# Kernel tuning notes

Hardware: AMD Instinct MI355X
Metric: run time of the kernel (lower is better)

The kernel has to match this reference:

```python
import jax, jax.numpy as jnp
import numpy as np

EMBED_DIM = 1024
BATCH = 4
SEQ = 2048


def setup_inputs() -> dict:
    key = jax.random.key(0)
    ks = jax.random.split(key, 9)
    E = EMBED_DIM
    s = 1.0 / np.sqrt(E)
    inp = {
        "x": jax.random.normal(ks[0], (BATCH, SEQ, E), dtype=jnp.float32),
        "Wq": jax.random.uniform(ks[1], (E, E), jnp.float32, -s, s),
        "bq": jax.random.uniform(ks[2], (E,), jnp.float32, -s, s),
        "Wk": jax.random.uniform(ks[3], (E, E), jnp.float32, -s, s),
        "bk": jax.random.uniform(ks[4], (E,), jnp.float32, -s, s),
        "Wv": jax.random.uniform(ks[5], (E, E), jnp.float32, -s, s),
        "bv": jax.random.uniform(ks[6], (E,), jnp.float32, -s, s),
        "Wo": jax.random.uniform(ks[7], (E, E), jnp.float32, -s, s),
        "bo": jax.random.uniform(ks[8], (E,), jnp.float32, -s, s),
    }
    return inp


def reference(x, Wq, bq, Wk, bk, Wv, bv, Wo, bo):
    # x: [B, S, E]. Single-head attention over full embed_dim.
    scale = x.shape[-1] ** -0.5
    q = jnp.einsum("bse,ef->bsf", x, Wq.T) + bq
    k = jnp.einsum("bse,ef->bsf", x, Wk.T) + bk
    v = jnp.einsum("bse,ef->bsf", x, Wv.T) + bv
    scores = jnp.einsum("bqe,bke->bqk", q, k) * scale  # [B, S, S]
    attn = jax.nn.softmax(scores, axis=-1)             # dropout p=0 -> identity
    out = jnp.einsum("bqk,bke->bqe", attn, v)
    return jnp.einsum("bse,ef->bsf", out, Wo.T) + bo
```

## Files before the change

kernel.cpp:

```cpp
#include <hip/hip_runtime.h>
#include <hip/hip_bf16.h>


typedef __bf16 bf16_t;
typedef __bf16 bf16x8 __attribute__((ext_vector_type(8)));
typedef __bf16 bf16x4 __attribute__((ext_vector_type(4)));
typedef float  f32x16 __attribute__((ext_vector_type(16)));
typedef float  f32x4  __attribute__((ext_vector_type(4)));

__device__ __forceinline__ void async_copy16(const void* g, void* l) {
  __builtin_amdgcn_global_load_lds(
      (const __attribute__((address_space(1))) void*)g,
      (__attribute__((address_space(3))) void*)l, 16, 0, 0);
}

__device__ __forceinline__ void wg_barrier() {
  asm volatile("" ::: "memory");
  __builtin_amdgcn_s_barrier();
  asm volatile("" ::: "memory");
}

__device__ __forceinline__ unsigned lds_addr(const void* p) {
  return (unsigned)(unsigned long long)(__attribute__((address_space(3))) const void*)p;
}

__device__ __forceinline__ bf16x8 ds_read128(const bf16_t* p) {
  bf16x8 r;
  asm volatile("ds_read_b128 %0, %1" : "=v"(r) : "v"(lds_addr(p)));
  return r;
}

__device__ __forceinline__ f32x4 mfma16(bf16x8 a, bf16x8 b, f32x4 c) {
  return __builtin_amdgcn_mfma_f32_16x16x32_bf16(a, b, c, 0, 0, 0);
}

__device__ __forceinline__ void store_out(float* p, float v)  { *p = v; }
__device__ __forceinline__ void store_out(bf16_t* p, float v) { *p = (bf16_t)v; }

#define BM 128
#define BN 128
#define BKT 64

template <typename OutT, int NBIAS>
__global__ __launch_bounds__(512, 2) void gemm256_bt(
    const bf16_t* __restrict__ A, const bf16_t* __restrict__ B,
    OutT* __restrict__ C,
    const float* __restrict__ b0, const float* __restrict__ b1,
    const float* __restrict__ b2,
    int M, int N, int K, int lda, int ldb, int ldc, float scale,
    long long strideA, long long strideB, long long strideC) {
  const int z = blockIdx.z;
  A += (long long)z * strideA;
  B += (long long)z * strideB;
  C += (long long)z * strideC;

  int bx = blockIdx.x, by = blockIdx.y;
  {
    const int GX  = gridDim.x;
    const int id  = by * GX + bx;
    const int per = GX * 8;
    const int grp = id / per;
    const int rem = id - grp * per;
    by = grp * 8 + (rem & 7);
    bx = rem >> 3;
  }

  __shared__ __align__(16) bf16_t As[2 * 256 * 64];
  __shared__ __align__(16) bf16_t Bs[2 * 256 * 64];

  const int t    = threadIdx.x;
  const int lane = t & 63;
  const int w    = t >> 6;
  const int wm   = w & 1;
  const int wn   = w >> 1;
  const int g    = lane >> 4;
  const int l7   = lane & 7;
  const int r15  = lane & 15;
  const int tileM = by * 256;
  const int tileN = bx * 256;

  const int row0 = t >> 3;
  const int gcc  = (t & 7) ^ (row0 & 7);
  const int dstb = (t & ~63) * 8;

  const int sw0 = ((0 + g) ^ l7) * 8;
  const int sw1 = ((4 + g) ^ l7) * 8;
  const int aRow = (wm * 128 + r15) * 64;
  const int bRow = (wn * 64 + r15) * 64;

  const int NT = K >> 6;

  f32x4 acc[8][4] = {};

  auto stageA = [&](int kt, int h) {
    const int cb = (kt & 1) * 16384;
    const bf16_t* src =
        A + (long long)(tileM + h * 128 + row0) * lda + kt * 64 + gcc * 8;
    bf16_t* dst = &As[cb + h * 8192 + dstb];
    async_copy16(src, dst);
    async_copy16(src + (long long)64 * lda, dst + 4096);
  };
  auto stageB = [&](int kt, int h) {
    const int cb = (kt & 1) * 16384;
    const bf16_t* src =
        B + (long long)(tileN + h * 128 + row0) * ldb + kt * 64 + gcc * 8;
    bf16_t* dst = &Bs[cb + h * 8192 + dstb];
    async_copy16(src, dst);
    async_copy16(src + (long long)64 * ldb, dst + 4096);
  };

  stageA(0, 0); stageA(0, 1); stageB(0, 0); stageB(0, 1);
  stageA(1, 0); stageA(1, 1); stageB(1, 0); stageB(1, 1);
  asm volatile("s_waitcnt vmcnt(8)" ::: "memory");
  wg_barrier();

  bf16x8 a[4][2], bq[2][2][2];

  for (int kt = 0; kt < NT; ++kt) {
    const int cb = (kt & 1) * 16384;
    const int k2 = kt + 2;
    const bf16_t* Ab = &As[cb + aRow];
    const bf16_t* Bb = &Bs[cb + bRow];

#pragma unroll
    for (int i = 0; i < 4; ++i) {
      a[i][0] = ds_read128(Ab + i * 1024 + sw0);
      a[i][1] = ds_read128(Ab + i * 1024 + sw1);
    }
#pragma unroll
    for (int j = 0; j < 2; ++j) {
      bq[0][j][0] = ds_read128(Bb + j * 1024 + sw0);
      bq[0][j][1] = ds_read128(Bb + j * 1024 + sw1);
    }
    wg_barrier();
    asm volatile("s_waitcnt lgkmcnt(0)");
    __builtin_amdgcn_sched_barrier(0);
    __builtin_amdgcn_s_setprio(1);
#pragma unroll
    for (int i = 0; i < 4; ++i)
#pragma unroll
      for (int j = 0; j < 2; ++j) {
        acc[i][j] = mfma16(a[i][0], bq[0][j][0], acc[i][j]);
        acc[i][j] = mfma16(a[i][1], bq[0][j][1], acc[i][j]);
      }
    __builtin_amdgcn_s_setprio(0);
    wg_barrier();

#pragma unroll
    for (int j = 0; j < 2; ++j) {
      bq[1][j][0] = ds_read128(Bb + 2048 + j * 1024 + sw0);
      bq[1][j][1] = ds_read128(Bb + 2048 + j * 1024 + sw1);
    }
    wg_barrier();
    asm volatile("s_waitcnt lgkmcnt(0)");
    __builtin_amdgcn_sched_barrier(0);
    __builtin_amdgcn_s_setprio(1);
#pragma unroll
    for (int i = 0; i < 4; ++i)
#pragma unroll
      for (int j = 0; j < 2; ++j) {
        acc[i][2 + j] = mfma16(a[i][0], bq[1][j][0], acc[i][2 + j]);
        acc[i][2 + j] = mfma16(a[i][1], bq[1][j][1], acc[i][2 + j]);
      }
    __builtin_amdgcn_s_setprio(0);
    wg_barrier();

#pragma unroll
    for (int i = 0; i < 4; ++i) {
      a[i][0] = ds_read128(Ab + 4096 + i * 1024 + sw0);
      a[i][1] = ds_read128(Ab + 4096 + i * 1024 + sw1);
    }
    if (k2 < NT) { stageB(k2, 0); stageB(k2, 1); }
    wg_barrier();
    asm volatile("s_waitcnt lgkmcnt(0)");
    __builtin_amdgcn_sched_barrier(0);
    __builtin_amdgcn_s_setprio(1);
#pragma unroll
    for (int i = 0; i < 4; ++i)
#pragma unroll
      for (int j = 0; j < 2; ++j) {
        acc[4 + i][2 + j] = mfma16(a[i][0], bq[1][j][0], acc[4 + i][2 + j]);
        acc[4 + i][2 + j] = mfma16(a[i][1], bq[1][j][1], acc[4 + i][2 + j]);
      }
    __builtin_amdgcn_s_setprio(0);
    wg_barrier();

    if (k2 < NT) { stageA(k2, 0); stageA(k2, 1); }
    __builtin_amdgcn_s_setprio(1);
#pragma unroll
    for (int i = 0; i < 4; ++i)
#pragma unroll
      for (int j = 0; j < 2; ++j) {
        acc[4 + i][j] = mfma16(a[i][0], bq[0][j][0], acc[4 + i][j]);
        acc[4 + i][j] = mfma16(a[i][1], bq[0][j][1], acc[4 + i][j]);
      }
    __builtin_amdgcn_s_setprio(0);
    if (k2 < NT) asm volatile("s_waitcnt vmcnt(8)" ::: "memory");
    else         asm volatile("s_waitcnt vmcnt(0)" ::: "memory");
    wg_barrier();
  }

  float bvv[4];
#pragma unroll
  for (int j = 0; j < 4; ++j) {
    const int col = tileN + wn * 64 + j * 16 + r15;
    float bv = 0.f;
    if (NBIAS == 1) bv = b0[col];
    if (NBIAS == 3) {
      const float* bp = col < 1024 ? b0 : (col < 2048 ? b1 : b2);
      bv = bp[col & 1023];
    }
    bvv[j] = bv;
  }
#pragma unroll
  for (int i = 0; i < 8; ++i) {
#pragma unroll
    for (int r = 0; r < 4; ++r) {
      const long long row = tileM + wm * 128 + i * 16 + g * 4 + r;
      OutT* Crow = C + row * ldc + tileN + wn * 64 + r15;
#pragma unroll
      for (int j = 0; j < 4; ++j)
        store_out(Crow + j * 16, acc[i][j][r] * scale + bvv[j]);
    }
  }
}

template <typename OutT, int NBIAS>
__global__ __launch_bounds__(256) void gemm_bt(
    const bf16_t* __restrict__ A, const bf16_t* __restrict__ B,
    OutT* __restrict__ C,
    const float* __restrict__ b0, const float* __restrict__ b1,
    const float* __restrict__ b2,
    int M, int N, int K, int lda, int ldb, int ldc, float scale,
    long long strideA, long long strideB, long long strideC) {
  const int z = blockIdx.z;
  A += (long long)z * strideA;
  B += (long long)z * strideB;
  C += (long long)z * strideC;

  int bx = blockIdx.x, by = blockIdx.y;
  {
    const int GX  = gridDim.x;
    const int id  = by * GX + bx;
    const int per = GX * 8;
    const int grp = id / per;
    const int rem = id - grp * per;
    by = grp * 8 + (rem & 7);
    bx = rem >> 3;
  }

  __shared__ __align__(16) bf16_t As[BM * BKT];
  __shared__ __align__(16) bf16_t Bs[BN * BKT];

  const int t    = threadIdx.x;
  const int lane = t & 63;
  const int w    = t >> 6;
  const int wm   = w & 1;
  const int wn   = w >> 1;
  const int tileM = by * BM;
  const int tileN = bx * BN;

  f32x16 acc[2][2] = {};

  for (int k0 = 0; k0 < K; k0 += BKT) {
#pragma unroll
    for (int i = 0; i < 4; ++i) {
      const int c   = t + 256 * i;
      const int row = c >> 3;
      const int cc  = c & 7;
      const int gcc = cc ^ (row & 7);
      const int ldsbase = ((t & ~63) + 256 * i) * 8;
      async_copy16(A + (long long)(tileM + row) * lda + k0 + gcc * 8, &As[ldsbase]);
      async_copy16(B + (long long)(tileN + row) * ldb + k0 + gcc * 8, &Bs[ldsbase]);
    }
    __syncthreads();

#pragma unroll
    for (int s = 0; s < 4; ++s) {
      const int kc = s + 4 * (lane >> 5);
      bf16x8 af[2], bfr[2];
#pragma unroll
      for (int ti = 0; ti < 2; ++ti) {
        const int row = wm * 64 + ti * 32 + (lane & 31);
        af[ti] = *(const bf16x8*)&As[row * BKT + ((kc ^ (row & 7)) * 8)];
      }
#pragma unroll
      for (int tj = 0; tj < 2; ++tj) {
        const int row = wn * 64 + tj * 32 + (lane & 31);
        bfr[tj] = *(const bf16x8*)&Bs[row * BKT + ((kc ^ (row & 7)) * 8)];
      }
#pragma unroll
      for (int ti = 0; ti < 2; ++ti)
#pragma unroll
        for (int tj = 0; tj < 2; ++tj)
          acc[ti][tj] = __builtin_amdgcn_mfma_f32_32x32x16_bf16(
              af[ti], bfr[tj], acc[ti][tj], 0, 0, 0);
    }
    __syncthreads();
  }

#pragma unroll
  for (int tj = 0; tj < 2; ++tj) {
    const int col = tileN + wn * 64 + tj * 32 + (lane & 31);
    float bv = 0.f;
    if (NBIAS == 1) bv = b0[col];
    if (NBIAS == 3) {
      const float* bp = col < 1024 ? b0 : (col < 2048 ? b1 : b2);
      bv = bp[col & 1023];
    }
#pragma unroll
    for (int ti = 0; ti < 2; ++ti) {
      const int rowb = tileM + wm * 64 + ti * 32 + 4 * (lane >> 5);
#pragma unroll
      for (int r = 0; r < 16; ++r) {
        const int row = rowb + (r & 3) + 8 * (r >> 2);
        store_out(&C[(long long)row * ldc + col], acc[ti][tj][r] * scale + bv);
      }
    }
  }
}

__global__ __launch_bounds__(256) void cast_all(
    const float4* __restrict__ w0, const float4* __restrict__ w1,
    const float4* __restrict__ w2, const float4* __restrict__ w3,
    const float4* __restrict__ x,
    bf16x4* __restrict__ wdst, bf16x4* __restrict__ xdst) {
  const int N4W = 1 << 18;
  const int id = blockIdx.x * 256 + threadIdx.x;
  const float4* src;
  bf16x4* dst;
  if (id < 4 * N4W) {
    const int z = id >> 18;
    src = (z == 0 ? w0 : z == 1 ? w1 : z == 2 ? w2 : w3) + (id & (N4W - 1));
    dst = wdst + id;
  } else {
    const int i = id - 4 * N4W;
    src = x + i;
    dst = xdst + i;
  }
  const float4 v = *src;
  bf16x4 o;
  o[0] = (bf16_t)v.x; o[1] = (bf16_t)v.y; o[2] = (bf16_t)v.z; o[3] = (bf16_t)v.w;
  *dst = o;
}

__global__ __launch_bounds__(256) void transpose_bf16(
    const bf16_t* __restrict__ in, bf16_t* __restrict__ out, int R, int C,
    int ldin, long long sIn, long long sOut) {
  in  += (long long)blockIdx.z * sIn;
  out += (long long)blockIdx.z * sOut;
  __shared__ bf16_t tile[32][33];
  const int tx = threadIdx.x, ty = threadIdx.y;
  const int x = blockIdx.x * 32 + tx;
  const int y0 = blockIdx.y * 32;
#pragma unroll
  for (int j = 0; j < 32; j += 8)
    tile[ty + j][tx] = in[(long long)(y0 + ty + j) * ldin + x];
  __syncthreads();
  const int x2 = y0 + tx;
  const int y2 = blockIdx.x * 32;
#pragma unroll
  for (int j = 0; j < 32; j += 8)
    out[(long long)(y2 + ty + j) * R + x2] = tile[tx][ty + j];
}

__global__ __launch_bounds__(256) void softmax_rows(
    const bf16_t* __restrict__ S, bf16_t* __restrict__ P, int cols) {
  const long long row = blockIdx.x;
  const bf16x8* inp = (const bf16x8*)(S + row * cols);
  bf16x8* outp      = (bf16x8*)(P + row * cols);
  const int t = threadIdx.x;
  const int w = t >> 6, lane = t & 63;

  const bf16x8 v = inp[t];
  float f[8];
#pragma unroll
  for (int j = 0; j < 8; ++j) f[j] = (float)v[j];

  float m = f[0];
#pragma unroll
  for (int j = 1; j < 8; ++j) m = fmaxf(m, f[j]);
#pragma unroll
  for (int off = 32; off > 0; off >>= 1) m = fmaxf(m, __shfl_xor(m, off));

  __shared__ float red[8];
  if (lane == 0) red[w] = m;
  __syncthreads();
  m = fmaxf(fmaxf(red[0], red[1]), fmaxf(red[2], red[3]));

  float e[8], sum = 0.f;
#pragma unroll
  for (int j = 0; j < 8; ++j) { e[j] = __expf(f[j] - m); sum += e[j]; }
#pragma unroll
  for (int off = 32; off > 0; off >>= 1) sum += __shfl_xor(sum, off);
  if (lane == 0) red[4 + w] = sum;
  __syncthreads();
  sum = red[4] + red[5] + red[6] + red[7];

  const float inv = 1.f / sum;
  bf16x8 o;
#pragma unroll
  for (int j = 0; j < 8; ++j) o[j] = (bf16_t)(e[j] * inv);
  outp[t] = o;
}

extern "C" void kernel_launch(void* const* d_in, const int* in_sizes, int n_in,
                              void* d_out, int out_size, void* d_ws, size_t ws_size,
                              hipStream_t stream) {
  const int E = 1024, S = 2048, B = 4;
  const int BS = B * S;

  const float* x  = (const float*)d_in[0];
  const float* Wq = (const float*)d_in[1];
  const float* bq = (const float*)d_in[2];
  const float* Wk = (const float*)d_in[3];
  const float* bk = (const float*)d_in[4];
  const float* Wv = (const float*)d_in[5];
  const float* bv = (const float*)d_in[6];
  const float* Wo = (const float*)d_in[7];
  const float* bo = (const float*)d_in[8];
  float* out = (float*)d_out;

  char* w = (char*)d_ws;
  const size_t MB = 1ull << 20;
  bf16_t* Wqkvb = (bf16_t*)(w + 0 * MB);
  bf16_t* Wob   = Wqkvb + 3 * E * E;
  bf16_t* xb    = (bf16_t*)(w + 8 * MB);
  bf16_t* QKVb  = (bf16_t*)(w + 24 * MB);
  bf16_t* VTb   = (bf16_t*)(w + 72 * MB);
  bf16_t* Sb    = (bf16_t*)(w + 88 * MB);
  bf16_t* Pb    = (bf16_t*)(w + 8 * MB);
  bf16_t* Ob    = (bf16_t*)(w + 40 * MB);

  {
    const int totalBlocks = ((4 << 18) + (1 << 21)) / 256;
    cast_all<<<totalBlocks, 256, 0, stream>>>(
        (const float4*)Wq, (const float4*)Wk, (const float4*)Wv,
        (const float4*)Wo, (const float4*)x, (bf16x4*)Wqkvb, (bf16x4*)xb);
  }

  gemm256_bt<bf16_t, 3><<<dim3(3 * E / 256, BS / 256, 1), 512, 0, stream>>>(
      xb, Wqkvb, QKVb, bq, bk, bv,
      BS, 3 * E, E, E, E, 3 * E, 1.f, 0, 0, 0);

  transpose_bf16<<<dim3(E / 32, S / 32, B), dim3(32, 8), 0, stream>>>(
      QKVb + 2 * E, VTb, S, E, 3 * E, (long long)S * 3 * E, (long long)E * S);

  gemm256_bt<bf16_t, 0><<<dim3(S / 256, S / 256, B), 512, 0, stream>>>(
      QKVb, QKVb + E, Sb, nullptr, nullptr, nullptr,
      S, S, E, 3 * E, 3 * E, S, 0.03125f,
      (long long)S * 3 * E, (long long)S * 3 * E, (long long)S * S);

  softmax_rows<<<BS, 256, 0, stream>>>(Sb, Pb, S);

  gemm_bt<bf16_t, 0><<<dim3(E / BN, S / BM, B), 256, 0, stream>>>(
      Pb, VTb, Ob, nullptr, nullptr, nullptr,
      S, E, S, S, S, E, 1.f,
      (long long)S * S, (long long)E * S, (long long)S * E);

  gemm_bt<float, 1><<<dim3(E / BN, BS / BM, 1), 256, 0, stream>>>(
      Ob, Wob, out, bo, nullptr, nullptr,
      BS, E, E, E, E, E, 1.f, 0, 0, 0);
}
```

Before: 292.5 us.

## Prefetch next tile's B fragments during last MFMA phase via ping-pong registers

Restructures the GEMM main loop so the B fragments for the next k-tile are read from LDS during the final MFMA quadrant of the current tile. Two register sets are alternated by unrolling the loop by two. The vmcnt wait moves earlier (vmcnt(4)) and the prologue stage order changes so the B tile lands first. MFMA issue is also reordered by k-slice. The goal is to hide LDS read latency and remove one barrier-delimited phase per tile. In exchange it raises register pressure, and it assumes NT is even.

```diff
diff --git a/kernel.cpp b/kernel.cpp
--- a/kernel.cpp
+++ b/kernel.cpp
@@ -18,6 +18,11 @@
   asm volatile("" ::: "memory");
   __builtin_amdgcn_s_barrier();
   asm volatile("" ::: "memory");
+}
+
+__device__ __forceinline__ void lgkm0_fence() {
+  asm volatile("s_waitcnt lgkmcnt(0)" ::: "memory");
+  __builtin_amdgcn_sched_barrier(0);
 }
 
 __device__ __forceinline__ unsigned lds_addr(const void* p) {
@@ -110,13 +115,19 @@
   };
 
   stageA(0, 0); stageA(0, 1); stageB(0, 0); stageB(0, 1);
-  stageA(1, 0); stageA(1, 1); stageB(1, 0); stageB(1, 1);
+  stageB(1, 0); stageB(1, 1); stageA(1, 0); stageA(1, 1);
   asm volatile("s_waitcnt vmcnt(8)" ::: "memory");
   wg_barrier();
 
-  bf16x8 a[4][2], bq[2][2][2];
-
-  for (int kt = 0; kt < NT; ++kt) {
+  bf16x8 a[4][2], P[2][2], Q[2][2];
+
+#pragma unroll
+  for (int j = 0; j < 2; ++j) {
+    P[j][0] = ds_read128(&Bs[bRow + j * 1024 + sw0]);
+    P[j][1] = ds_read128(&Bs[bRow + j * 1024 + sw1]);
+  }
+
+  auto tile_step = [&](int kt, bf16x8 (&bc)[2][2], bf16x8 (&bq)[2][2]) {
     const int cb = (kt & 1) * 16384;
     const int k2 = kt + 2;
     const bf16_t* Ab = &As[cb + aRow];
@@ -127,41 +138,34 @@
       a[i][0] = ds_read128(Ab + i * 1024 + sw0);
       a[i][1] = ds_read128(Ab + i * 1024 + sw1);
     }
+    wg_barrier();
+    lgkm0_fence();
+    __builtin_amdgcn_s_setprio(1);
+#pragma unroll
+    for (int s = 0; s < 2; ++s)
+#pragma unroll
+      for (int i = 0; i < 4; ++i)
+#pragma unroll
+        for (int j = 0; j < 2; ++j)
+          acc[i][j] = mfma16(a[i][s], bc[j][s], acc[i][j]);
+    __builtin_amdgcn_s_setprio(0);
+    wg_barrier();
+
 #pragma unroll
     for (int j = 0; j < 2; ++j) {
-      bq[0][j][0] = ds_read128(Bb + j * 1024 + sw0);
-      bq[0][j][1] = ds_read128(Bb + j * 1024 + sw1);
-    }
-    wg_barrier();
-    asm volatile("s_waitcnt lgkmcnt(0)");
-    __builtin_amdgcn_sched_barrier(0);
+      bq[j][0] = ds_read128(Bb + 2048 + j * 1024 + sw0);
+      bq[j][1] = ds_read128(Bb + 2048 + j * 1024 + sw1);
+    }
+    wg_barrier();
+    lgkm0_fence();
     __builtin_amdgcn_s_setprio(1);
 #pragma unroll
-    for (int i = 0; i < 4; ++i)
-#pragma unroll
-      for (int j = 0; j < 2; ++j) {
-        acc[i][j] = mfma16(a[i][0], bq[0][j][0], acc[i][j]);
-        acc[i][j] = mfma16(a[i][1], bq[0][j][1], acc[i][j]);
-      }
-    __builtin_amdgcn_s_setprio(0);
-    wg_barrier();
-
-#pragma unroll
-    for (int j = 0; j < 2; ++j) {
-      bq[1][j][0] = ds_read128(Bb + 2048 + j * 1024 + sw0);
-      bq[1][j][1] = ds_read128(Bb + 2048 + j * 1024 + sw1);
-    }
-    wg_barrier();
-    asm volatile("s_waitcnt lgkmcnt(0)");
-    __builtin_amdgcn_sched_barrier(0);
-    __builtin_amdgcn_s_setprio(1);
-#pragma unroll
-    for (int i = 0; i < 4; ++i)
-#pragma unroll
-      for (int j = 0; j < 2; ++j) {
-        acc[i][2 + j] = mfma16(a[i][0], bq[1][j][0], acc[i][2 + j]);
-        acc[i][2 + j] = mfma16(a[i][1], bq[1][j][1], acc[i][2 + j]);
-      }
+    for (int s = 0; s < 2; ++s)
+#pragma unroll
+      for (int i = 0; i < 4; ++i)
+#pragma unroll
+        for (int j = 0; j < 2; ++j)
+          acc[i][2 + j] = mfma16(a[i][s], bq[j][s], acc[i][2 + j]);
     __builtin_amdgcn_s_setprio(0);
     wg_barrier();
 
@@ -172,32 +176,44 @@
     }
     if (k2 < NT) { stageB(k2, 0); stageB(k2, 1); }
     wg_barrier();
-    asm volatile("s_waitcnt lgkmcnt(0)");
-    __builtin_amdgcn_sched_barrier(0);
+    lgkm0_fence();
     __builtin_amdgcn_s_setprio(1);
 #pragma unroll
-    for (int i = 0; i < 4; ++i)
+    for (int s = 0; s < 2; ++s)
+#pragma unroll
+      for (int i = 0; i < 4; ++i)
+#pragma unroll
+        for (int j = 0; j < 2; ++j)
+          acc[4 + i][2 + j] = mfma16(a[i][s], bq[j][s], acc[4 + i][2 + j]);
+    __builtin_amdgcn_s_setprio(0);
+    if (k2 < NT) asm volatile("s_waitcnt vmcnt(4)" ::: "memory");
+    else         asm volatile("s_waitcnt vmcnt(0)" ::: "memory");
+    wg_barrier();
+
+    if (kt + 1 < NT) {
+      const bf16_t* Bn = &Bs[((kt + 1) & 1) * 16384 + bRow];
 #pragma unroll
       for (int j = 0; j < 2; ++j) {
-        acc[4 + i][2 + j] = mfma16(a[i][0], bq[1][j][0], acc[4 + i][2 + j]);
-        acc[4 + i][2 + j] = mfma16(a[i][1], bq[1][j][1], acc[4 + i][2 + j]);
+        bq[j][0] = ds_read128(Bn + j * 1024 + sw0);
+        bq[j][1] = ds_read128(Bn + j * 1024 + sw1);
       }
-    __builtin_amdgcn_s_setprio(0);
-    wg_barrier();
-
+    }
     if (k2 < NT) { stageA(k2, 0); stageA(k2, 1); }
     __builtin_amdgcn_s_setprio(1);
 #pragma unroll
-    for (int i = 0; i < 4; ++i)
-#pragma unroll
-      for (int j = 0; j < 2; ++j) {
-        acc[4 + i][j] = mfma16(a[i][0], bq[0][j][0], acc[4 + i][j]);
-        acc[4 + i][j] = mfma16(a[i][1], bq[0][j][1], acc[4 + i][j]);
-      }
+    for (int s = 0; s < 2; ++s)
+#pragma unroll
+      for (int i = 0; i < 4; ++i)
+#pragma unroll
+        for (int j = 0; j < 2; ++j)
+          acc[4 + i][j] = mfma16(a[i][s], bc[j][s], acc[4 + i][j]);
     __builtin_amdgcn_s_setprio(0);
-    if (k2 < NT) asm volatile("s_waitcnt vmcnt(8)" ::: "memory");
-    else         asm volatile("s_waitcnt vmcnt(0)" ::: "memory");
-    wg_barrier();
+    wg_barrier();
+  };
+
+  for (int kt = 0; kt < NT; kt += 2) {
+    tile_step(kt,     P, Q);
+    tile_step(kt + 1, Q, P);
   }
 
   float bvv[4];
```

Result: no change. 296.1 us (+1.2%).
